# Kernel tuning notes

Measured on AMD Instinct MI355X. Metric: run time of the kernel, lower is better.

Reference implementation:

```python
import jax, jax.numpy as jnp
import numpy as np

N, E, D, H = 20000, 320000, 300, 2
NEG_SLOPE = 0.2  # PyG GATConv default LeakyReLU slope


def setup_inputs() -> dict:
    key = jax.random.key(0)
    ks = jax.random.split(key, 8)
    return {
        "x": jax.random.normal(ks[0], (N, D), dtype=jnp.float32),
        "edge_index": jax.random.randint(ks[1], (2, E), 0, N, dtype=jnp.int64),
        "W": jax.random.normal(ks[2], (D, H, D), dtype=jnp.float32) * 0.05,
        "att_src": jax.random.normal(ks[3], (H, D), dtype=jnp.float32) * 0.05,
        "att_dst": jax.random.normal(ks[4], (H, D), dtype=jnp.float32) * 0.05,
        "bias": jax.random.normal(ks[5], (D,), dtype=jnp.float32) * 0.05,
        "lin_w": jax.random.normal(ks[6], (D, 1), dtype=jnp.float32) * 0.05,
        "lin_b": jax.random.normal(ks[7], (1,), dtype=jnp.float32) * 0.05,
    }


def reference(x, edge_index, W, att_src, att_dst, bias, lin_w, lin_b):
    n = x.shape[0]
    # add self-loops (PyG GATConv default)
    loops = jnp.arange(n, dtype=edge_index.dtype)
    src = jnp.concatenate([edge_index[0], loops])  # [E+N]
    dst = jnp.concatenate([edge_index[1], loops])
    # per-head linear projection: [N, H, D]
    xp = jnp.einsum('nd,dhe->nhe', x, W)
    # per-node attention logits [N, H]
    a_src = jnp.sum(xp * att_src, axis=-1)
    a_dst = jnp.sum(xp * att_dst, axis=-1)
    # per-edge score, LeakyReLU, segment softmax over incoming edges of dst
    e = jax.nn.leaky_relu(a_src[src] + a_dst[dst], NEG_SLOPE)  # [Et, H]
    emax = jax.ops.segment_max(e, dst, num_segments=n)  # self-loops ensure non-empty
    ee = jnp.exp(e - emax[dst])
    denom = jax.ops.segment_sum(ee, dst, num_segments=n)
    alpha = ee / denom[dst]  # [Et, H]
    # weighted scatter-add aggregation
    msg = xp[src] * alpha[:, :, None]  # [Et, H, D]
    out = jax.ops.segment_sum(msg, dst, num_segments=n)  # [N, H, D]
    out = out.mean(axis=1) + bias  # concat=False -> head average, then bias
    out = jax.nn.relu(out)
    return out @ lin_w + lin_b  # [N, 1]
```

## Files before the change

kernel.cpp:

```cpp
#include <hip/hip_runtime.h>
#include <math.h>

#define Nn 20000
#define Ee 320000
#define Dd 300
#define Hh 2
#define Cc 600
#define KP 320
#define MP 20096
#define NP 640
#define SQ 640

typedef _Float16 f16;
typedef __attribute__((ext_vector_type(8))) _Float16 f16x8;
typedef __attribute__((ext_vector_type(4))) _Float16 f16x4;
typedef __attribute__((ext_vector_type(4))) float f32x4;

__device__ __forceinline__ float lrelu(float x) { return x > 0.f ? x : 0.2f * x; }

#define GLDS16(src, dst)                                                            \
  __builtin_amdgcn_global_load_lds(                                                 \
      (const __attribute__((address_space(1))) unsigned int*)(src),                 \
      (__attribute__((address_space(3))) unsigned int*)(dst), 16, 0, 0)

__global__ __launch_bounds__(256) void k_pre2(const float* __restrict__ W,
                                              const float* __restrict__ att_src,
                                              const float* __restrict__ att_dst,
                                              f16* __restrict__ Wh, float* __restrict__ vatt,
                                              int* __restrict__ cnt) {
  int idx = blockIdx.x * 256 + threadIdx.x;
  if (idx < Nn) cnt[idx] = 0;
  {
    int c = idx % NP, k0 = (idx / NP) * 4;
    f16x4 h;
#pragma unroll
    for (int j = 0; j < 4; ++j) {
      int k = k0 + j;
      h[j] = (f16)((k < Dd && c < Cc) ? W[(size_t)k * Cc + c] : 0.f);
    }
    *(f16x4*)(Wh + (size_t)c * KP + k0) = h;
  }
  int wid = idx >> 6, ln = idx & 63;
  if (wid < Dd) {
    float s0 = 0.f, s1 = 0.f, t0 = 0.f, t1 = 0.f;
    for (int e = ln; e < Dd; e += 64) {
      float w0 = W[(size_t)wid * Cc + e];
      float w1 = W[(size_t)wid * Cc + Dd + e];
      s0 += w0 * att_src[e];  s1 += w1 * att_src[Dd + e];
      t0 += w0 * att_dst[e];  t1 += w1 * att_dst[Dd + e];
    }
    for (int o = 32; o > 0; o >>= 1) {
      s0 += __shfl_down(s0, o, 64); s1 += __shfl_down(s1, o, 64);
      t0 += __shfl_down(t0, o, 64); t1 += __shfl_down(t1, o, 64);
    }
    if (ln == 0) {
      vatt[wid * 4 + 0] = s0; vatt[wid * 4 + 1] = s1;
      vatt[wid * 4 + 2] = t0; vatt[wid * 4 + 3] = t1;
    }
  }
}

__global__ __launch_bounds__(256) void k_pre1(const float* __restrict__ x,
                                              const float* __restrict__ vatt,
                                              const int* __restrict__ ei,
                                              f16* __restrict__ xh,
                                              float* __restrict__ a_src, float* __restrict__ a_dst,
                                              int* __restrict__ cnt) {
  int gid = blockIdx.x * 256 + threadIdx.x;
  if (gid < Ee) atomicAdd(&cnt[ei[Ee + gid]], 1);
  int wv = threadIdx.x >> 6, ln = threadIdx.x & 63;
  int n = blockIdx.x * 4 + wv;
  if (n >= MP) return;
  if (n >= Nn) {
#pragma unroll
    for (int k = 0; k < 5; ++k) xh[(size_t)n * KP + ln + 64 * k] = (f16)0.f;
    return;
  }
  const float* xr = x + (size_t)n * Dd;
  float s0 = 0.f, s1 = 0.f, t0 = 0.f, t1 = 0.f;
#pragma unroll
  for (int k = 0; k < 5; ++k) {
    int d = ln + 64 * k;
    float xv = 0.f;
    if (d < Dd) {
      xv = xr[d];
      float4 vv = *(const float4*)(vatt + d * 4);
      s0 += xv * vv.x; s1 += xv * vv.y; t0 += xv * vv.z; t1 += xv * vv.w;
    }
    xh[(size_t)n * KP + d] = (f16)xv;
  }
  for (int o = 32; o > 0; o >>= 1) {
    s0 += __shfl_down(s0, o, 64); s1 += __shfl_down(s1, o, 64);
    t0 += __shfl_down(t0, o, 64); t1 += __shfl_down(t1, o, 64);
  }
  if (ln == 0) {
    a_src[n * 2 + 0] = s0; a_src[n * 2 + 1] = s1;
    a_dst[n * 2 + 0] = t0; a_dst[n * 2 + 1] = t1;
  }
}

__global__ __launch_bounds__(256) void k_mm(const f16* __restrict__ xh, const f16* __restrict__ Wh,
                                            f16* __restrict__ xq) {
  __shared__ __align__(16) f16 As[128 * 32];
  __shared__ __align__(16) f16 Bs[128 * 32];
  int m0 = blockIdx.x * 128, n0 = blockIdx.y * 128;
  int tid = threadIdx.x, wv = tid >> 6, lane = tid & 63;
  int wr = wv >> 1, wc = wv & 1;

  int r0a = 32 * wv + (lane >> 2);
  int ca  = ((lane & 3) ^ ((r0a >> 1) & 3)) * 8;
  int r0b = r0a + 16;
  int cb  = ((lane & 3) ^ ((r0b >> 1) & 3)) * 8;

  f32x4 acc[4][4] = {};
  for (int ks = 0; ks < KP / 32; ++ks) {
    __syncthreads();
    GLDS16(xh + (size_t)(m0 + r0a) * KP + ks * 32 + ca, As + (32 * wv) * 32);
    GLDS16(xh + (size_t)(m0 + r0b) * KP + ks * 32 + cb, As + (32 * wv + 16) * 32);
    GLDS16(Wh + (size_t)(n0 + r0a) * KP + ks * 32 + ca, Bs + (32 * wv) * 32);
    GLDS16(Wh + (size_t)(n0 + r0b) * KP + ks * 32 + cb, Bs + (32 * wv + 16) * 32);
    __syncthreads();

    f16x8 af[4], bf[4];
#pragma unroll
    for (int i = 0; i < 4; ++i) {
      int rA = wr * 64 + i * 16 + (lane & 15);
      int sA = (lane >> 4) ^ ((rA >> 1) & 3);
      af[i] = *(const f16x8*)&As[rA * 32 + sA * 8];
      int rB = wc * 64 + i * 16 + (lane & 15);
      int sB = (lane >> 4) ^ ((rB >> 1) & 3);
      bf[i] = *(const f16x8*)&Bs[rB * 32 + sB * 8];
    }
#pragma unroll
    for (int i = 0; i < 4; ++i)
#pragma unroll
      for (int j = 0; j < 4; ++j)
        acc[i][j] = __builtin_amdgcn_mfma_f32_16x16x32_f16(af[i], bf[j], acc[i][j], 0, 0, 0);
  }

#pragma unroll
  for (int i = 0; i < 4; ++i) {
#pragma unroll
    for (int j = 0; j < 4; ++j) {
      int col = n0 + wc * 64 + j * 16 + (lane & 15);
      if (col < Cc) {
        int rbase = m0 + wr * 64 + i * 16 + ((lane >> 4) * 4);
#pragma unroll
        for (int r = 0; r < 4; ++r) {
          int row = rbase + r;
          if (row < Nn) xq[(size_t)row * SQ + col] = (f16)acc[i][j][r];
        }
      }
    }
  }
}

__global__ __launch_bounds__(1024) void k_scan(const int* __restrict__ cnt,
                                               int* __restrict__ offs, int* __restrict__ cur) {
  __shared__ int wsum[16];
  int t = threadIdx.x, wv = t >> 6, ln = t & 63;
  int i0 = t * 20;
  int v[20];
  int tot = 0;
  if (i0 < Nn) {
    const int4* p = (const int4*)(cnt + i0);
#pragma unroll
    for (int q = 0; q < 5; ++q) {
      int4 w = p[q];
      v[4 * q] = w.x; v[4 * q + 1] = w.y; v[4 * q + 2] = w.z; v[4 * q + 3] = w.w;
    }
#pragma unroll
    for (int j = 0; j < 20; ++j) tot += v[j];
  }
  int s = tot;
  for (int o = 1; o < 64; o <<= 1) {
    int u = __shfl_up(s, o, 64);
    if (ln >= o) s += u;
  }
  if (ln == 63) wsum[wv] = s;
  __syncthreads();
  if (wv == 0) {
    int w = (ln < 16) ? wsum[ln] : 0;
    for (int o = 1; o < 16; o <<= 1) {
      int u = __shfl_up(w, o, 64);
      if (ln >= o) w += u;
    }
    if (ln < 16) wsum[ln] = w;
  }
  __syncthreads();
  if (i0 < Nn) {
    int run = (wv > 0 ? wsum[wv - 1] : 0) + (s - tot);
#pragma unroll
    for (int j = 0; j < 20; ++j) {
      offs[i0 + j] = run;
      cur[i0 + j] = run;
      run += v[j];
    }
  }
  if (t == 0) offs[Nn] = wsum[15];
}

__global__ void k_scatter(const int* __restrict__ ei, int* __restrict__ cur,
                          int* __restrict__ srt) {
  int e = blockIdx.x * 256 + threadIdx.x;
  if (e < Ee) {
    int s = ei[e], d = ei[Ee + e];
    int pos = atomicAdd(&cur[d], 1);
    srt[pos] = s;
  }
}

__global__ __launch_bounds__(256) void k_agg(const f16* __restrict__ xq,
    const float* __restrict__ a_src, const float* __restrict__ a_dst,
    const int* __restrict__ offs, const int* __restrict__ srt,
    const float* __restrict__ bias, const float* __restrict__ lin_w,
    const float* __restrict__ lin_b, float* __restrict__ out) {
  __shared__ float sAgg[4][600];
  int tid = threadIdx.x, wv = tid >> 6, ln = tid & 63;
  int n = blockIdx.x * 4 + wv;
  int beg = offs[n], deg = offs[n + 1] - beg;
  float2 adv = *(const float2*)(a_dst + 2 * n);
  float2 asv = *(const float2*)(a_src + 2 * n);
  float se0 = lrelu(asv.x + adv.x), se1 = lrelu(asv.y + adv.y);
  float sw0 = __expf(se0), sw1 = __expf(se1);

  float acc[12] = {};
  auto addrow = [&](const f16* row, float p0, float p1) {
#pragma unroll
    for (int k = 0; k < 3; ++k) {
      int c = 4 * ln + 256 * k;
      if (c < Cc) {
        f16x4 hv = *(const f16x4*)(row + c);
        float p = (c < Dd) ? p0 : p1;
        acc[4 * k + 0] += p * (float)hv[0];
        acc[4 * k + 1] += p * (float)hv[1];
        acc[4 * k + 2] += p * (float)hv[2];
        acc[4 * k + 3] += p * (float)hv[3];
      }
    }
  };

  if (deg <= 64) {
    int ss = -1; float e0 = 0.f, e1 = 0.f;
    if (ln < deg) {
      int s = srt[beg + ln];
      float2 av = *(const float2*)(a_src + 2 * s);
      ss = s;
      e0 = __expf(lrelu(av.x + adv.x));
      e1 = __expf(lrelu(av.y + adv.y));
    }
    float t0 = e0, t1 = e1;
    for (int o = 32; o > 0; o >>= 1) {
      t0 += __shfl_xor(t0, o, 64);
      t1 += __shfl_xor(t1, o, 64);
    }
    float inv0 = 1.f / (t0 + sw0), inv1 = 1.f / (t1 + sw1);
    float p0 = e0 * inv0, p1 = e1 * inv1;
#pragma unroll 4
    for (int j = 0; j < deg; ++j) {
      int s = __shfl(ss, j, 64);
      float q0 = __shfl(p0, j, 64), q1 = __shfl(p1, j, 64);
      addrow(xq + (size_t)s * SQ, q0, q1);
    }
    addrow(xq + (size_t)n * SQ, sw0 * inv0, sw1 * inv1);
  } else {
    float t0 = 0.f, t1 = 0.f;
    for (int base = 0; base < deg; base += 64) {
      if (ln < deg - base) {
        int s = srt[beg + base + ln];
        float2 av = *(const float2*)(a_src + 2 * s);
        t0 += __expf(lrelu(av.x + adv.x));
        t1 += __expf(lrelu(av.y + adv.y));
      }
    }
    for (int o = 32; o > 0; o >>= 1) {
      t0 += __shfl_xor(t0, o, 64);
      t1 += __shfl_xor(t1, o, 64);
    }
    float inv0 = 1.f / (t0 + sw0), inv1 = 1.f / (t1 + sw1);
    for (int base = 0; base < deg; base += 64) {
      int cnt2 = min(64, deg - base);
      float p0 = 0.f, p1 = 0.f; int s2 = -1;
      if (ln < cnt2) {
        int s = srt[beg + base + ln];
        float2 av = *(const float2*)(a_src + 2 * s);
        s2 = s;
        p0 = __expf(lrelu(av.x + adv.x)) * inv0;
        p1 = __expf(lrelu(av.y + adv.y)) * inv1;
      }
#pragma unroll 4
      for (int j = 0; j < cnt2; ++j) {
        int s = __shfl(s2, j, 64);
        float q0 = __shfl(p0, j, 64), q1 = __shfl(p1, j, 64);
        addrow(xq + (size_t)s * SQ, q0, q1);
      }
    }
    addrow(xq + (size_t)n * SQ, sw0 * inv0, sw1 * inv1);
  }

#pragma unroll
  for (int k = 0; k < 3; ++k) {
    int c = 4 * ln + 256 * k;
    if (c < Cc) {
#pragma unroll
      for (int j = 0; j < 4; ++j) sAgg[wv][c + j] = acc[4 * k + j];
    }
  }
  __syncthreads();

  float part = 0.f;
#pragma unroll
  for (int k = 0; k < 5; ++k) {
    int d = ln + 64 * k;
    if (d < Dd) {
      float v = 0.5f * (sAgg[wv][d] + sAgg[wv][d + Dd]) + bias[d];
      v = fmaxf(v, 0.f);
      part += v * lin_w[d];
    }
  }
  for (int o = 32; o > 0; o >>= 1) part += __shfl_xor(part, o, 64);
  if (ln == 0) out[n] = part + lin_b[0];
}

extern "C" void kernel_launch(void* const* d_in, const int* in_sizes, int n_in,
                              void* d_out, int out_size, void* d_ws, size_t ws_size,
                              hipStream_t stream) {
  const float* x       = (const float*)d_in[0];
  const int*   ei      = (const int*)d_in[1];
  const float* W       = (const float*)d_in[2];
  const float* att_src = (const float*)d_in[3];
  const float* att_dst = (const float*)d_in[4];
  const float* bias    = (const float*)d_in[5];
  const float* lin_w   = (const float*)d_in[6];
  const float* lin_b   = (const float*)d_in[7];
  float* out = (float*)d_out;

  char* ws = (char*)d_ws;
  size_t off = 0;
  auto alloc = [&](size_t bytes) {
    void* p = ws + off;
    off = (off + bytes + 255) & ~(size_t)255;
    return p;
  };
  f16*   xq    = (f16*)alloc((size_t)Nn * SQ * 2);
  f16*   xh    = (f16*)alloc((size_t)MP * KP * 2);
  f16*   Wh    = (f16*)alloc((size_t)NP * KP * 2);
  float* vatt  = (float*)alloc((size_t)Dd * 4 * 4);
  float* a_src = (float*)alloc((size_t)Nn * Hh * 4);
  float* a_dst = (float*)alloc((size_t)Nn * Hh * 4);
  int*   cnt   = (int*)alloc((size_t)Nn * 4);
  int*   offs  = (int*)alloc((size_t)(Nn + 1) * 4);
  int*   cur   = (int*)alloc((size_t)Nn * 4);
  int*   srt   = (int*)alloc((size_t)Ee * 4);

  k_pre2<<<NP * (KP / 4) / 256, 256, 0, stream>>>(W, att_src, att_dst, Wh, vatt, cnt);
  k_pre1<<<MP / 4, 256, 0, stream>>>(x, vatt, ei, xh, a_src, a_dst, cnt);
  k_mm<<<dim3(MP / 128, NP / 128), 256, 0, stream>>>(xh, Wh, xq);
  k_scan<<<1, 1024, 0, stream>>>(cnt, offs, cur);
  k_scatter<<<(Ee + 255) / 256, 256, 0, stream>>>(ei, cur, srt);
  k_agg<<<Nn / 4, 256, 0, stream>>>(xq, a_src, a_dst, offs, srt, bias, lin_w, lin_b, out);
}
```

Before: 214.3 us.

## Precompute edge attention weights and softmax denominators during CSR scatter

The scatter kernel now computes exp(leaky_relu) edge scores for both heads and writes them, together with the source index, as a 16-byte record per edge. It also accumulates per-destination denominators with float atomics. The aggregation kernel reads these records directly and drops its own gathers of a_src, its exp work and its wave reductions, which leaves a simple unrolled loop over edges. In exchange the scatter does extra atomics and writes four times the per-edge data, and the float atomic sums are nondeterministic.

```diff
diff --git a/kernel.cpp b/kernel.cpp
--- a/kernel.cpp
+++ b/kernel.cpp
@@ -27,9 +27,12 @@
                                               const float* __restrict__ att_src,
                                               const float* __restrict__ att_dst,
                                               f16* __restrict__ Wh, float* __restrict__ vatt,
-                                              int* __restrict__ cnt) {
+                                              int* __restrict__ cnt, float* __restrict__ dsum) {
   int idx = blockIdx.x * 256 + threadIdx.x;
-  if (idx < Nn) cnt[idx] = 0;
+  if (idx < Nn) {
+    cnt[idx] = 0;
+    *(float2*)(dsum + 2 * idx) = make_float2(0.f, 0.f);
+  }
   {
     int c = idx % NP, k0 = (idx / NP) * 4;
     f16x4 h;
@@ -200,19 +203,28 @@
   if (t == 0) offs[Nn] = wsum[15];
 }
 
-__global__ void k_scatter(const int* __restrict__ ei, int* __restrict__ cur,
-                          int* __restrict__ srt) {
+__global__ void k_scatter(const int* __restrict__ ei,
+                          const float* __restrict__ a_src, const float* __restrict__ a_dst,
+                          int* __restrict__ cur, float* __restrict__ dsum,
+                          float4* __restrict__ erec) {
   int e = blockIdx.x * 256 + threadIdx.x;
   if (e < Ee) {
     int s = ei[e], d = ei[Ee + e];
+    float2 av = *(const float2*)(a_src + 2 * s);
+    float2 bv = *(const float2*)(a_dst + 2 * d);
+    float e0 = __expf(lrelu(av.x + bv.x));
+    float e1 = __expf(lrelu(av.y + bv.y));
     int pos = atomicAdd(&cur[d], 1);
-    srt[pos] = s;
+    erec[pos] = make_float4(__int_as_float(s), e0, e1, 0.f);
+    atomicAdd(&dsum[2 * d + 0], e0);
+    atomicAdd(&dsum[2 * d + 1], e1);
   }
 }
 
 __global__ __launch_bounds__(256) void k_agg(const f16* __restrict__ xq,
+    const float4* __restrict__ erec,
     const float* __restrict__ a_src, const float* __restrict__ a_dst,
-    const int* __restrict__ offs, const int* __restrict__ srt,
+    const float* __restrict__ dsum, const int* __restrict__ offs,
     const float* __restrict__ bias, const float* __restrict__ lin_w,
     const float* __restrict__ lin_b, float* __restrict__ out) {
   __shared__ float sAgg[4][600];
@@ -221,8 +233,10 @@
   int beg = offs[n], deg = offs[n + 1] - beg;
   float2 adv = *(const float2*)(a_dst + 2 * n);
   float2 asv = *(const float2*)(a_src + 2 * n);
-  float se0 = lrelu(asv.x + adv.x), se1 = lrelu(asv.y + adv.y);
-  float sw0 = __expf(se0), sw1 = __expf(se1);
+  float sw0 = __expf(lrelu(asv.x + adv.x));
+  float sw1 = __expf(lrelu(asv.y + adv.y));
+  float2 dv = *(const float2*)(dsum + 2 * n);
+  float inv0 = 1.f / (dv.x + sw0), inv1 = 1.f / (dv.y + sw1);
 
   float acc[12] = {};
   auto addrow = [&](const f16* row, float p0, float p1) {
@@ -240,70 +254,29 @@
     }
   };
 
-  if (deg <= 64) {
-    int ss = -1; float e0 = 0.f, e1 = 0.f;
-    if (ln < deg) {
-      int s = srt[beg + ln];
-      float2 av = *(const float2*)(a_src + 2 * s);
-      ss = s;
-      e0 = __expf(lrelu(av.x + adv.x));
-      e1 = __expf(lrelu(av.y + adv.y));
-    }
-    float t0 = e0, t1 = e1;
-    for (int o = 32; o > 0; o >>= 1) {
-      t0 += __shfl_xor(t0, o, 64);
-      t1 += __shfl_xor(t1, o, 64);
-    }
-    float inv0 = 1.f / (t0 + sw0), inv1 = 1.f / (t1 + sw1);
-    float p0 = e0 * inv0, p1 = e1 * inv1;
-#pragma unroll 4
-    for (int j = 0; j < deg; ++j) {
-      int s = __shfl(ss, j, 64);
-      float q0 = __shfl(p0, j, 64), q1 = __shfl(p1, j, 64);
-      addrow(xq + (size_t)s * SQ, q0, q1);
-    }
-    addrow(xq + (size_t)n * SQ, sw0 * inv0, sw1 * inv1);
-  } else {
-    float t0 = 0.f, t1 = 0.f;
-    for (int base = 0; base < deg; base += 64) {
-      if (ln < deg - base) {
-        int s = srt[beg + base + ln];
-        float2 av = *(const float2*)(a_src + 2 * s);
-        t0 += __expf(lrelu(av.x + adv.x));
-        t1 += __expf(lrelu(av.y + adv.y));
-      }
-    }
-    for (int o = 32; o > 0; o >>= 1) {
-      t0 += __shfl_xor(t0, o, 64);
-      t1 += __shfl_xor(t1, o, 64);
-    }
-    float inv0 = 1.f / (t0 + sw0), inv1 = 1.f / (t1 + sw1);
-    for (int base = 0; base < deg; base += 64) {
-      int cnt2 = min(64, deg - base);
-      float p0 = 0.f, p1 = 0.f; int s2 = -1;
-      if (ln < cnt2) {
-        int s = srt[beg + base + ln];
-        float2 av = *(const float2*)(a_src + 2 * s);
-        s2 = s;
-        p0 = __expf(lrelu(av.x + adv.x)) * inv0;
-        p1 = __expf(lrelu(av.y + adv.y)) * inv1;
-      }
-#pragma unroll 4
-      for (int j = 0; j < cnt2; ++j) {
-        int s = __shfl(s2, j, 64);
-        float q0 = __shfl(p0, j, 64), q1 = __shfl(p1, j, 64);
-        addrow(xq + (size_t)s * SQ, q0, q1);
-      }
-    }
-    addrow(xq + (size_t)n * SQ, sw0 * inv0, sw1 * inv1);
-  }
+  int j = 0;
+  for (; j + 4 <= deg; j += 4) {
+    float4 r0 = erec[beg + j + 0];
+    float4 r1 = erec[beg + j + 1];
+    float4 r2 = erec[beg + j + 2];
+    float4 r3 = erec[beg + j + 3];
+    addrow(xq + (size_t)__float_as_int(r0.x) * SQ, r0.y * inv0, r0.z * inv1);
+    addrow(xq + (size_t)__float_as_int(r1.x) * SQ, r1.y * inv0, r1.z * inv1);
+    addrow(xq + (size_t)__float_as_int(r2.x) * SQ, r2.y * inv0, r2.z * inv1);
+    addrow(xq + (size_t)__float_as_int(r3.x) * SQ, r3.y * inv0, r3.z * inv1);
+  }
+  for (; j < deg; ++j) {
+    float4 r = erec[beg + j];
+    addrow(xq + (size_t)__float_as_int(r.x) * SQ, r.y * inv0, r.z * inv1);
+  }
+  addrow(xq + (size_t)n * SQ, sw0 * inv0, sw1 * inv1);
 
 #pragma unroll
   for (int k = 0; k < 3; ++k) {
     int c = 4 * ln + 256 * k;
     if (c < Cc) {
 #pragma unroll
-      for (int j = 0; j < 4; ++j) sAgg[wv][c + j] = acc[4 * k + j];
+      for (int q = 0; q < 4; ++q) sAgg[wv][c + q] = acc[4 * k + q];
     }
   }
   __syncthreads();
@@ -342,21 +315,22 @@
     off = (off + bytes + 255) & ~(size_t)255;
     return p;
   };
-  f16*   xq    = (f16*)alloc((size_t)Nn * SQ * 2);
-  f16*   xh    = (f16*)alloc((size_t)MP * KP * 2);
-  f16*   Wh    = (f16*)alloc((size_t)NP * KP * 2);
-  float* vatt  = (float*)alloc((size_t)Dd * 4 * 4);
-  float* a_src = (float*)alloc((size_t)Nn * Hh * 4);
-  float* a_dst = (float*)alloc((size_t)Nn * Hh * 4);
-  int*   cnt   = (int*)alloc((size_t)Nn * 4);
-  int*   offs  = (int*)alloc((size_t)(Nn + 1) * 4);
-  int*   cur   = (int*)alloc((size_t)Nn * 4);
-  int*   srt   = (int*)alloc((size_t)Ee * 4);
-
-  k_pre2<<<NP * (KP / 4) / 256, 256, 0, stream>>>(W, att_src, att_dst, Wh, vatt, cnt);
+  f16*    xq    = (f16*)alloc((size_t)Nn * SQ * 2);
+  f16*    xh    = (f16*)alloc((size_t)MP * KP * 2);
+  f16*    Wh    = (f16*)alloc((size_t)NP * KP * 2);
+  float*  vatt  = (float*)alloc((size_t)Dd * 4 * 4);
+  float*  a_src = (float*)alloc((size_t)Nn * Hh * 4);
+  float*  a_dst = (float*)alloc((size_t)Nn * Hh * 4);
+  int*    cnt   = (int*)alloc((size_t)Nn * 4);
+  int*    offs  = (int*)alloc((size_t)(Nn + 1) * 4);
+  int*    cur   = (int*)alloc((size_t)Nn * 4);
+  float*  dsum  = (float*)alloc((size_t)Nn * 2 * 4);
+  float4* erec  = (float4*)alloc((size_t)Ee * 16);
+
+  k_pre2<<<NP * (KP / 4) / 256, 256, 0, stream>>>(W, att_src, att_dst, Wh, vatt, cnt, dsum);
   k_pre1<<<MP / 4, 256, 0, stream>>>(x, vatt, ei, xh, a_src, a_dst, cnt);
   k_mm<<<dim3(MP / 128, NP / 128), 256, 0, stream>>>(xh, Wh, xq);
   k_scan<<<1, 1024, 0, stream>>>(cnt, offs, cur);
-  k_scatter<<<(Ee + 255) / 256, 256, 0, stream>>>(ei, cur, srt);
-  k_agg<<<Nn / 4, 256, 0, stream>>>(xq, a_src, a_dst, offs, srt, bias, lin_w, lin_b, out);
-}
+  k_scatter<<<(Ee + 255) / 256, 256, 0, stream>>>(ei, a_src, a_dst, cur, dsum, erec);
+  k_agg<<<Nn / 4, 256, 0, stream>>>(xq, erec, a_src, a_dst, dsum, offs, bias, lin_w, lin_b, out);
+}
```

Result: slower. 246.8 us (+15.2%).
